# Optimization experiments

Measured on AMD Instinct MI355X. Metric: run time of the kernel, lower is better.

## Reference

```python
import jax, jax.numpy as jnp
import numpy as np

FILTERS = 256
KERNEL = 3
B, C, W = 8, 256, 8192
# he_std = gain / sqrt(fan_in) with fan_in = kernel_size * in_dim, lrmul = 1
RUNTIME_COEF = 1.0 / np.sqrt(KERNEL * C)


def setup_inputs() -> dict:
    key = jax.random.key(0)
    k1, k2, k3 = jax.random.split(key, 3)
    feature = jax.random.normal(k1, (B, C, W), dtype=jnp.float32)
    style = jax.random.normal(k2, (B, C), dtype=jnp.float32)
    kernel = jax.random.normal(k3, (KERNEL, C, FILTERS), dtype=jnp.float32)
    return {"feature": feature, "style": style, "kernel": kernel}


def reference(feature, style, kernel):
    b, c, w = feature.shape
    kk, _, f = kernel.shape
    # modulate: per-sample weights [B, k, C, F]
    weights = (kernel * RUNTIME_COEF)[None, ...] * (style[:, None, :, None] + 1.0)
    # demodulate: normalize over (k, C) per (B, F)
    denom = jax.lax.rsqrt(jnp.sum(jnp.square(weights), axis=(1, 2), keepdims=True))
    weights = weights * denom
    # batch-as-groups conv1d: lhs [1, B*C, W], rhs [k, C, B*F], groups = B
    lhs = feature.reshape(1, b * c, w)
    rhs = jnp.transpose(weights, (1, 2, 0, 3)).reshape(kk, c, b * f)
    out = jax.lax.conv_general_dilated(
        lhs, rhs,
        window_strides=(1,),
        padding="SAME",
        dimension_numbers=("NCH", "HIO", "NCH"),
        feature_group_count=b,
    )  # [1, B*F, W]
    return out.reshape(b, f, -1)
```

## Files before the change

### kernel.cpp

```cpp
#include <hip/hip_runtime.h>

#define B_   8
#define C_   256
#define W_   8192
#define F_   256
#define KK   3
#define KC   768
#define WP   (W_ + 2)
#define COEF 0.03608439182435161f

#define BN_   256
#define BKc   64
#define NT    12
#define ABASE 0
#define BBASE 16384
#define BUFU  32768

using f32x16 = __attribute__((ext_vector_type(16))) float;
using bf16x8 = __attribute__((ext_vector_type(8))) __bf16;

#define AS1(p) ((const __attribute__((address_space(1))) void*)(p))
#define AS3(p) ((__attribute__((address_space(3))) void*)(p))

__device__ __forceinline__ unsigned short f2bf(float x) {
    union { float f; unsigned int u; } v; v.f = x;
    unsigned int u = v.u;
    u += 0x7FFFu + ((u >> 16) & 1u);
    return (unsigned short)(u >> 16);
}

__global__ __launch_bounds__(256) void prep_w(const float* __restrict__ kern,
                                              const float* __restrict__ style,
                                              unsigned short* __restrict__ kT,
                                              float* __restrict__ denom,
                                              unsigned short* __restrict__ featT) {
    __shared__ float sst[C_];
    if (blockIdx.x < B_) {
        const int b = blockIdx.x, f = threadIdx.x;
        sst[f] = (style[b * C_ + f] + 1.0f) * COEF;
        __syncthreads();
        float sum = 0.f;
#pragma unroll 16
        for (int kc = 0; kc < KC; ++kc) {
            float w = kern[(size_t)kc * F_ + f] * sst[kc & 255];
            sum += w * w;
        }
        denom[b * F_ + f] = rsqrtf(sum);
    } else {
        const int idx = (blockIdx.x - B_) * 256 + threadIdx.x;
        const int f = idx & 255, kc = idx >> 8;
        kT[(size_t)f * KC + kc] = f2bf(kern[idx] * COEF);
        if (idx < 4096) {
            const int b = idx >> 9, r = (idx >> 8) & 1, c = idx & 255;
            const size_t row = r ? (size_t)(WP - 1) : 0;
            featT[((size_t)b * WP + row) * C_ + c] = 0;
        }
    }
}

__global__ __launch_bounds__(256) void prep_featT(const float* __restrict__ feat,
                                                  const float* __restrict__ style,
                                                  unsigned short* __restrict__ featT) {
    __shared__ float tile[64][65];
    const int tid = threadIdx.x;
    const int b = blockIdx.z, c0 = blockIdx.y * 64, w0 = blockIdx.x * 64;

    const int x4 = tid & 15, cl4 = tid >> 4;
#pragma unroll
    for (int p = 0; p < 4; ++p) {
        const int cl = cl4 + p * 16;
        const float s = style[b * C_ + c0 + cl] + 1.0f;
        float4 v = *(const float4*)(feat + ((size_t)b * C_ + c0 + cl) * W_ + w0 + x4 * 4);
        tile[x4 * 4 + 0][cl] = v.x * s;
        tile[x4 * 4 + 1][cl] = v.y * s;
        tile[x4 * 4 + 2][cl] = v.z * s;
        tile[x4 * 4 + 3][cl] = v.w * s;
    }
    __syncthreads();

    const int ch = tid & 7, wr = tid >> 3;
#pragma unroll
    for (int p = 0; p < 2; ++p) {
        const int w = wr + p * 32;
        unsigned int pk[4];
#pragma unroll
        for (int j = 0; j < 4; ++j) {
            float v0 = tile[w][ch * 8 + 2 * j];
            float v1 = tile[w][ch * 8 + 2 * j + 1];
            pk[j] = (unsigned int)f2bf(v0) | ((unsigned int)f2bf(v1) << 16);
        }
        uint4 u; u.x = pk[0]; u.y = pk[1]; u.z = pk[2]; u.w = pk[3];
        *(uint4*)(featT + ((size_t)b * WP + (w0 + w + 1)) * C_ + c0 + ch * 8) = u;
    }
}

__global__ __launch_bounds__(512, 2) void conv_mod(
        const unsigned short* __restrict__ featT,
        const unsigned short* __restrict__ kT,
        const float* __restrict__ denom,
        float* __restrict__ out) {
    __shared__ __align__(16) unsigned short ring[2 * BUFU];

    const int tid  = threadIdx.x;
    const int b    = blockIdx.y;
    const int w0   = blockIdx.x * BN_;
    const int lane = tid & 63, wave = tid >> 6;
    const int wm   = (wave >> 2) * 128;
    const int wn   = (wave & 3) * 64;
    const int la   = lane & 31, kq = lane >> 5;

    const int srow = tid >> 3;
    const int sswz = ((tid & 7) ^ (srow & 7)) * 8;
    const unsigned short* aS0 = kT + (size_t)srow * KC + sswz;
    const unsigned short* bS0 = featT + ((size_t)b * WP + w0 + srow) * C_ + sswz;
    const int wdst = wave << 9;

    int ck[4];
#pragma unroll
    for (int kh = 0; kh < 4; ++kh) ck[kh] = ((kh * 2 + kq) ^ (la & 7)) * 8;
    const int ra = (wm + la) * BKc;
    const int rb = BBASE + (wn + la) * BKc;

    f32x16 acc[4][2] = {};

#define GLDS_A(g, kc, nb) __builtin_amdgcn_global_load_lds( \
        AS1(aS0 + (size_t)(g) * 64 * KC + (kc)), \
        AS3((nb) + ABASE + (g) * 4096 + wdst), 16, 0, 0)
#define GLDS_B(g, kc, nb) __builtin_amdgcn_global_load_lds( \
        AS1(bS0 + (size_t)(g) * 64 * C_ + (kc)), \
        AS3((nb) + BBASE + (g) * 4096 + wdst), 16, 0, 0)
#define PH_BAR() do { __builtin_amdgcn_s_barrier(); \
                      asm volatile("" ::: "memory"); } while (0)
#define VMW(n) do { __builtin_amdgcn_sched_barrier(0); \
                    asm volatile("s_waitcnt vmcnt(" #n ")" ::: "memory"); } while (0)

#define PHASE(MH, KH2) do { \
        bf16x8 av[2][2], bv[2][2]; \
        _Pragma("unroll") \
        for (int i = 0; i < 2; ++i) { \
            _Pragma("unroll") \
            for (int j = 0; j < 2; ++j) { \
                av[i][j] = *(const bf16x8*)&bf[ra + ((MH) * 2 + i) * 2048 + ck[(KH2) * 2 + j]]; \
                bv[i][j] = *(const bf16x8*)&bf[rb + i * 2048 + ck[(KH2) * 2 + j]]; \
            } \
        } \
        __builtin_amdgcn_s_setprio(1); \
        _Pragma("unroll") \
        for (int j = 0; j < 2; ++j) { \
            _Pragma("unroll") \
            for (int i = 0; i < 2; ++i) { \
                acc[(MH) * 2 + i][0] = __builtin_amdgcn_mfma_f32_32x32x16_bf16(av[i][j], bv[0][j], acc[(MH) * 2 + i][0], 0, 0, 0); \
                acc[(MH) * 2 + i][1] = __builtin_amdgcn_mfma_f32_32x32x16_bf16(av[i][j], bv[1][j], acc[(MH) * 2 + i][1], 0, 0, 0); \
            } \
        } \
        __builtin_amdgcn_s_setprio(0); \
    } while (0)

    {
        unsigned short* nb = ring;
        GLDS_A(0, 0, nb); GLDS_A(2, 0, nb);
        GLDS_B(0, 0, nb); GLDS_B(1, 0, nb);
        GLDS_B(2, 0, nb); GLDS_B(3, 0, nb);
        GLDS_A(1, 0, nb); GLDS_A(3, 0, nb);
    }
    VMW(2);
    PH_BAR();

#pragma unroll 1
    for (int t = 0; t < NT; ++t) {
        const unsigned short* bf = ring + (t & 1) * BUFU;
        unsigned short* nb = ring + ((t + 1) & 1) * BUFU;
        const int kn = (t < NT - 1 ? t + 1 : NT - 1) * BKc;

        GLDS_A(0, kn, nb); GLDS_A(2, kn, nb);
        GLDS_B(0, kn, nb); GLDS_B(1, kn, nb);
        PHASE(0, 0);
        PH_BAR();

        GLDS_B(2, kn, nb); GLDS_B(3, kn, nb);
        GLDS_A(1, kn, nb); GLDS_A(3, kn, nb);
        PHASE(0, 1);
        VMW(8);
        PH_BAR();

        PHASE(1, 0);
        PH_BAR();

        PHASE(1, 1);
        VMW(2);
        PH_BAR();
    }
    asm volatile("s_waitcnt vmcnt(0)" ::: "memory");

    const int bofs = b * F_;
    float* obase = out + (size_t)bofs * W_ + w0;
#pragma unroll
    for (int mi = 0; mi < 4; ++mi) {
#pragma unroll
        for (int r = 0; r < 16; ++r) {
            const int frow = (r & 3) + 8 * (r >> 2) + 4 * kq;
            const int f = wm + mi * 32 + frow;
            const float d = denom[bofs + f];
            float* orow = obase + (size_t)f * W_ + wn + la;
            orow[0]  = acc[mi][0][r] * d;
            orow[32] = acc[mi][1][r] * d;
        }
    }
#undef GLDS_A
#undef GLDS_B
#undef PH_BAR
#undef VMW
#undef PHASE
}

extern "C" void kernel_launch(void* const* d_in, const int* in_sizes, int n_in,
                              void* d_out, int out_size, void* d_ws, size_t ws_size,
                              hipStream_t stream) {
    const float* feature = (const float*)d_in[0];
    const float* style   = (const float*)d_in[1];
    const float* kern    = (const float*)d_in[2];
    float* out = (float*)d_out;

    unsigned short* kT    = (unsigned short*)d_ws;
    float*          denom = (float*)((char*)d_ws + (size_t)F_ * KC * 2);
    unsigned short* featT = (unsigned short*)((char*)d_ws + (size_t)F_ * KC * 2 + 8192);

    hipLaunchKernelGGL(prep_w,     dim3(KC + B_), dim3(256), 0, stream,
                       kern, style, kT, denom, featT);
    hipLaunchKernelGGL(prep_featT, dim3(W_ / 64, C_ / 64, B_), dim3(256), 0, stream,
                       feature, style, featT);
    hipLaunchKernelGGL(conv_mod,   dim3(W_ / BN_, B_), dim3(512), 0, stream,
                       featT, kT, denom, out);
}
```

Baseline: 170.3 us.

## Switch conv GEMM to 4-slot ring with BK=32 and prefetch distance 3

```diff
diff --git a/kernel.cpp b/kernel.cpp
--- a/kernel.cpp
+++ b/kernel.cpp
@@ -9,12 +9,11 @@
 #define WP   (W_ + 2)
 #define COEF 0.03608439182435161f
 
-#define BN_   256
-#define BKc   64
-#define NT    12
-#define ABASE 0
-#define BBASE 16384
-#define BUFU  32768
+#define BN_    256
+#define BKc    32
+#define NT     24
+#define SLOTU  16384
+#define BBASEU 8192
 
 using f32x16 = __attribute__((ext_vector_type(16))) float;
 using bf16x8 = __attribute__((ext_vector_type(8))) __bf16;
@@ -99,7 +98,7 @@
         const unsigned short* __restrict__ kT,
         const float* __restrict__ denom,
         float* __restrict__ out) {
-    __shared__ __align__(16) unsigned short ring[2 * BUFU];
+    __shared__ __align__(16) unsigned short ring[4 * SLOTU];
 
     const int tid  = threadIdx.x;
     const int b    = blockIdx.y;
@@ -109,86 +108,72 @@
     const int wn   = (wave & 3) * 64;
     const int la   = lane & 31, kq = lane >> 5;
 
-    const int srow = tid >> 3;
-    const int sswz = ((tid & 7) ^ (srow & 7)) * 8;
+    const int srow = tid >> 2;
+    const int sswz = ((tid & 3) ^ ((tid >> 3) & 3)) * 8;
     const unsigned short* aS0 = kT + (size_t)srow * KC + sswz;
     const unsigned short* bS0 = featT + ((size_t)b * WP + w0 + srow) * C_ + sswz;
     const int wdst = wave << 9;
 
-    int ck[4];
-#pragma unroll
-    for (int kh = 0; kh < 4; ++kh) ck[kh] = ((kh * 2 + kq) ^ (la & 7)) * 8;
-    const int ra = (wm + la) * BKc;
-    const int rb = BBASE + (wn + la) * BKc;
+    int ck2[2];
+#pragma unroll
+    for (int j = 0; j < 2; ++j) ck2[j] = ((j * 2 + kq) ^ ((la >> 1) & 3)) * 8;
+    const int ra0 = (wm + la) * BKc;
+    const int rb0 = BBASEU + (wn + la) * BKc;
 
     f32x16 acc[4][2] = {};
 
 #define GLDS_A(g, kc, nb) __builtin_amdgcn_global_load_lds( \
-        AS1(aS0 + (size_t)(g) * 64 * KC + (kc)), \
-        AS3((nb) + ABASE + (g) * 4096 + wdst), 16, 0, 0)
+        AS1(aS0 + (size_t)(g) * 128 * KC + (kc)), \
+        AS3((nb) + (g) * 4096 + wdst), 16, 0, 0)
 #define GLDS_B(g, kc, nb) __builtin_amdgcn_global_load_lds( \
-        AS1(bS0 + (size_t)(g) * 64 * C_ + (kc)), \
-        AS3((nb) + BBASE + (g) * 4096 + wdst), 16, 0, 0)
-#define PH_BAR() do { __builtin_amdgcn_s_barrier(); \
-                      asm volatile("" ::: "memory"); } while (0)
-#define VMW(n) do { __builtin_amdgcn_sched_barrier(0); \
-                    asm volatile("s_waitcnt vmcnt(" #n ")" ::: "memory"); } while (0)
-
-#define PHASE(MH, KH2) do { \
-        bf16x8 av[2][2], bv[2][2]; \
-        _Pragma("unroll") \
-        for (int i = 0; i < 2; ++i) { \
-            _Pragma("unroll") \
-            for (int j = 0; j < 2; ++j) { \
-                av[i][j] = *(const bf16x8*)&bf[ra + ((MH) * 2 + i) * 2048 + ck[(KH2) * 2 + j]]; \
-                bv[i][j] = *(const bf16x8*)&bf[rb + i * 2048 + ck[(KH2) * 2 + j]]; \
-            } \
-        } \
-        __builtin_amdgcn_s_setprio(1); \
-        _Pragma("unroll") \
-        for (int j = 0; j < 2; ++j) { \
-            _Pragma("unroll") \
-            for (int i = 0; i < 2; ++i) { \
-                acc[(MH) * 2 + i][0] = __builtin_amdgcn_mfma_f32_32x32x16_bf16(av[i][j], bv[0][j], acc[(MH) * 2 + i][0], 0, 0, 0); \
-                acc[(MH) * 2 + i][1] = __builtin_amdgcn_mfma_f32_32x32x16_bf16(av[i][j], bv[1][j], acc[(MH) * 2 + i][1], 0, 0, 0); \
-            } \
-        } \
-        __builtin_amdgcn_s_setprio(0); \
+        AS1(bS0 + (size_t)(g) * 128 * C_ + (kc)), \
+        AS3((nb) + BBASEU + (g) * 4096 + wdst), 16, 0, 0)
+#define STAGE(kc, nb) do { \
+        GLDS_A(0, kc, nb); GLDS_A(1, kc, nb); \
+        GLDS_B(0, kc, nb); GLDS_B(1, kc, nb); \
     } while (0)
 
-    {
-        unsigned short* nb = ring;
-        GLDS_A(0, 0, nb); GLDS_A(2, 0, nb);
-        GLDS_B(0, 0, nb); GLDS_B(1, 0, nb);
-        GLDS_B(2, 0, nb); GLDS_B(3, 0, nb);
-        GLDS_A(1, 0, nb); GLDS_A(3, 0, nb);
-    }
-    VMW(2);
-    PH_BAR();
+    STAGE(0 * BKc, ring);
+    STAGE(1 * BKc, ring + SLOTU);
+    STAGE(2 * BKc, ring + 2 * SLOTU);
+    __builtin_amdgcn_sched_barrier(0);
+    asm volatile("s_waitcnt vmcnt(8)" ::: "memory");
+    __builtin_amdgcn_s_barrier();
+    asm volatile("" ::: "memory");
 
 #pragma unroll 1
     for (int t = 0; t < NT; ++t) {
-        const unsigned short* bf = ring + (t & 1) * BUFU;
-        unsigned short* nb = ring + ((t + 1) & 1) * BUFU;
-        const int kn = (t < NT - 1 ? t + 1 : NT - 1) * BKc;
-
-        GLDS_A(0, kn, nb); GLDS_A(2, kn, nb);
-        GLDS_B(0, kn, nb); GLDS_B(1, kn, nb);
-        PHASE(0, 0);
-        PH_BAR();
-
-        GLDS_B(2, kn, nb); GLDS_B(3, kn, nb);
-        GLDS_A(1, kn, nb); GLDS_A(3, kn, nb);
-        PHASE(0, 1);
-        VMW(8);
-        PH_BAR();
-
-        PHASE(1, 0);
-        PH_BAR();
-
-        PHASE(1, 1);
-        VMW(2);
-        PH_BAR();
+        const unsigned short* bf = ring + (t & 3) * SLOTU;
+        unsigned short* nb = ring + ((t + 3) & 3) * SLOTU;
+        const int tn = (t + 3 < NT) ? t + 3 : NT - 1;
+
+        STAGE(tn * BKc, nb);
+
+        bf16x8 av[4][2], bv[2][2];
+#pragma unroll
+        for (int j = 0; j < 2; ++j) {
+#pragma unroll
+            for (int ni = 0; ni < 2; ++ni)
+                bv[ni][j] = *(const bf16x8*)&bf[rb0 + ni * 1024 + ck2[j]];
+#pragma unroll
+            for (int mi = 0; mi < 4; ++mi)
+                av[mi][j] = *(const bf16x8*)&bf[ra0 + mi * 1024 + ck2[j]];
+        }
+        __builtin_amdgcn_s_setprio(1);
+#pragma unroll
+        for (int j = 0; j < 2; ++j) {
+#pragma unroll
+            for (int mi = 0; mi < 4; ++mi) {
+                acc[mi][0] = __builtin_amdgcn_mfma_f32_32x32x16_bf16(av[mi][j], bv[0][j], acc[mi][0], 0, 0, 0);
+                acc[mi][1] = __builtin_amdgcn_mfma_f32_32x32x16_bf16(av[mi][j], bv[1][j], acc[mi][1], 0, 0, 0);
+            }
+        }
+        __builtin_amdgcn_s_setprio(0);
+
+        __builtin_amdgcn_sched_barrier(0);
+        asm volatile("s_waitcnt vmcnt(8)" ::: "memory");
+        __builtin_amdgcn_s_barrier();
+        asm volatile("" ::: "memory");
     }
     asm volatile("s_waitcnt vmcnt(0)" ::: "memory");
 
@@ -208,9 +193,7 @@
     }
 #undef GLDS_A
 #undef GLDS_B
-#undef PH_BAR
-#undef VMW
-#undef PHASE
+#undef STAGE
 }
 
 extern "C" void kernel_launch(void* const* d_in, const int* in_sizes, int n_in,
```

Result: no change. 170.1 us (-0.1%).

## Halve conv tile width, triple-buffer B tiles, and swizzle block order

Applied to the files above, without the earlier changes.

```diff
diff --git a/kernel.cpp b/kernel.cpp
--- a/kernel.cpp
+++ b/kernel.cpp
@@ -9,12 +9,12 @@
 #define WP   (W_ + 2)
 #define COEF 0.03608439182435161f
 
-#define BN_   256
-#define BKc   64
-#define NT    12
-#define ABASE 0
-#define BBASE 16384
-#define BUFU  32768
+#define BN_    128
+#define BKc    64
+#define NT     12
+#define ASLOTU 16384
+#define BBASEU 32768
+#define BSLOTU 8192
 
 using f32x16 = __attribute__((ext_vector_type(16))) float;
 using bf16x8 = __attribute__((ext_vector_type(8))) __bf16;
@@ -99,14 +99,16 @@
         const unsigned short* __restrict__ kT,
         const float* __restrict__ denom,
         float* __restrict__ out) {
-    __shared__ __align__(16) unsigned short ring[2 * BUFU];
+    __shared__ __align__(16) unsigned short ring[BBASEU + 3 * BSLOTU];
 
     const int tid  = threadIdx.x;
-    const int b    = blockIdx.y;
-    const int w0   = blockIdx.x * BN_;
+    const int lin  = blockIdx.y * 64 + blockIdx.x;
+    const int swz  = (lin & 7) * 64 + (lin >> 3);
+    const int b    = swz >> 6;
+    const int w0   = (swz & 63) * BN_;
     const int lane = tid & 63, wave = tid >> 6;
-    const int wm   = (wave >> 2) * 128;
-    const int wn   = (wave & 3) * 64;
+    const int wm   = (wave >> 1) * 64;
+    const int wn   = (wave & 1) * 64;
     const int la   = lane & 31, kq = lane >> 5;
 
     const int srow = tid >> 3;
@@ -118,84 +120,78 @@
     int ck[4];
 #pragma unroll
     for (int kh = 0; kh < 4; ++kh) ck[kh] = ((kh * 2 + kq) ^ (la & 7)) * 8;
-    const int ra = (wm + la) * BKc;
-    const int rb = BBASE + (wn + la) * BKc;
-
-    f32x16 acc[4][2] = {};
-
-#define GLDS_A(g, kc, nb) __builtin_amdgcn_global_load_lds( \
+    const int ra0 = (wm + la) * BKc;
+    const int rb0 = (wn + la) * BKc;
+
+    f32x16 acc[2][2] = {};
+
+#define GLDS_A(g, kc, sb) __builtin_amdgcn_global_load_lds( \
         AS1(aS0 + (size_t)(g) * 64 * KC + (kc)), \
-        AS3((nb) + ABASE + (g) * 4096 + wdst), 16, 0, 0)
-#define GLDS_B(g, kc, nb) __builtin_amdgcn_global_load_lds( \
+        AS3(ring + (sb) + (g) * 4096 + wdst), 16, 0, 0)
+#define GLDS_B(g, kc, sb) __builtin_amdgcn_global_load_lds( \
         AS1(bS0 + (size_t)(g) * 64 * C_ + (kc)), \
-        AS3((nb) + BBASE + (g) * 4096 + wdst), 16, 0, 0)
-#define PH_BAR() do { __builtin_amdgcn_s_barrier(); \
-                      asm volatile("" ::: "memory"); } while (0)
+        AS3(ring + BBASEU + (sb) + (g) * 4096 + wdst), 16, 0, 0)
+#define SBAR() do { __builtin_amdgcn_sched_barrier(0); \
+                    __builtin_amdgcn_s_barrier(); \
+                    asm volatile("" ::: "memory"); } while (0)
 #define VMW(n) do { __builtin_amdgcn_sched_barrier(0); \
                     asm volatile("s_waitcnt vmcnt(" #n ")" ::: "memory"); } while (0)
 
-#define PHASE(MH, KH2) do { \
+#define PHASE(Q) do { \
         bf16x8 av[2][2], bv[2][2]; \
         _Pragma("unroll") \
         for (int i = 0; i < 2; ++i) { \
             _Pragma("unroll") \
             for (int j = 0; j < 2; ++j) { \
-                av[i][j] = *(const bf16x8*)&bf[ra + ((MH) * 2 + i) * 2048 + ck[(KH2) * 2 + j]]; \
-                bv[i][j] = *(const bf16x8*)&bf[rb + i * 2048 + ck[(KH2) * 2 + j]]; \
+                av[i][j] = *(const bf16x8*)&ab[ra0 + i * 2048 + ck[(Q) * 2 + j]]; \
+                bv[i][j] = *(const bf16x8*)&bb[rb0 + i * 2048 + ck[(Q) * 2 + j]]; \
             } \
         } \
+        SBAR(); \
         __builtin_amdgcn_s_setprio(1); \
         _Pragma("unroll") \
         for (int j = 0; j < 2; ++j) { \
             _Pragma("unroll") \
             for (int i = 0; i < 2; ++i) { \
-                acc[(MH) * 2 + i][0] = __builtin_amdgcn_mfma_f32_32x32x16_bf16(av[i][j], bv[0][j], acc[(MH) * 2 + i][0], 0, 0, 0); \
-                acc[(MH) * 2 + i][1] = __builtin_amdgcn_mfma_f32_32x32x16_bf16(av[i][j], bv[1][j], acc[(MH) * 2 + i][1], 0, 0, 0); \
+                acc[i][0] = __builtin_amdgcn_mfma_f32_32x32x16_bf16(av[i][j], bv[0][j], acc[i][0], 0, 0, 0); \
+                acc[i][1] = __builtin_amdgcn_mfma_f32_32x32x16_bf16(av[i][j], bv[1][j], acc[i][1], 0, 0, 0); \
             } \
         } \
         __builtin_amdgcn_s_setprio(0); \
     } while (0)
 
-    {
-        unsigned short* nb = ring;
-        GLDS_A(0, 0, nb); GLDS_A(2, 0, nb);
-        GLDS_B(0, 0, nb); GLDS_B(1, 0, nb);
-        GLDS_B(2, 0, nb); GLDS_B(3, 0, nb);
-        GLDS_A(1, 0, nb); GLDS_A(3, 0, nb);
-    }
+    GLDS_A(0, 0, 0); GLDS_A(1, 0, 0); GLDS_A(2, 0, 0); GLDS_A(3, 0, 0);
+    GLDS_B(0, 0, 0); GLDS_B(1, 0, 0);
+    GLDS_B(0, BKc, BSLOTU); GLDS_B(1, BKc, BSLOTU);
     VMW(2);
-    PH_BAR();
+    __builtin_amdgcn_s_barrier();
+    asm volatile("" ::: "memory");
 
 #pragma unroll 1
     for (int t = 0; t < NT; ++t) {
-        const unsigned short* bf = ring + (t & 1) * BUFU;
-        unsigned short* nb = ring + ((t + 1) & 1) * BUFU;
-        const int kn = (t < NT - 1 ? t + 1 : NT - 1) * BKc;
-
-        GLDS_A(0, kn, nb); GLDS_A(2, kn, nb);
-        GLDS_B(0, kn, nb); GLDS_B(1, kn, nb);
-        PHASE(0, 0);
-        PH_BAR();
-
-        GLDS_B(2, kn, nb); GLDS_B(3, kn, nb);
-        GLDS_A(1, kn, nb); GLDS_A(3, kn, nb);
-        PHASE(0, 1);
-        VMW(8);
-        PH_BAR();
-
-        PHASE(1, 0);
-        PH_BAR();
-
-        PHASE(1, 1);
+        const unsigned short* ab = ring + (t & 1) * ASLOTU;
+        const unsigned short* bb = ring + BBASEU + (t % 3) * BSLOTU;
+        const int an = (t + 1 < NT ? t + 1 : NT - 1) * BKc;
+        const int bn = (t + 2 < NT ? t + 2 : NT - 1) * BKc;
+        const int as = ((t + 1) & 1) * ASLOTU;
+        const int bs = ((t + 2) % 3) * BSLOTU;
+
+        GLDS_A(0, an, as); GLDS_A(1, an, as);
+        GLDS_A(2, an, as); GLDS_A(3, an, as);
+        PHASE(0);
+        SBAR();
+
+        GLDS_B(0, bn, bs); GLDS_B(1, bn, bs);
+        PHASE(1);
         VMW(2);
-        PH_BAR();
+        SBAR();
     }
     asm volatile("s_waitcnt vmcnt(0)" ::: "memory");
 
     const int bofs = b * F_;
     float* obase = out + (size_t)bofs * W_ + w0;
 #pragma unroll
-    for (int mi = 0; mi < 4; ++mi) {
+    for (int mi = 0; mi < 2; ++mi) {
 #pragma unroll
         for (int r = 0; r < 16; ++r) {
             const int frow = (r & 3) + 8 * (r >> 2) + 4 * kq;
@@ -208,7 +204,7 @@
     }
 #undef GLDS_A
 #undef GLDS_B
-#undef PH_BAR
+#undef SBAR
 #undef VMW
 #undef PHASE
 }
```

Measured after the change: 172.3 us. About the same (+1.2%).
